# Kernel optimization log

Measured on AMD Instinct MI355X. Metric: run time of the kernel, lower is better.

Reference implementation:

```python
import jax, jax.numpy as jnp
import numpy as np

HALF_FEATURE_NUMEL = 49152  # 12 pieces * 64 squares * 64 king buckets
INTER_DIM = 768             # factorizer collapses king bucket: i % 768


def setup_inputs() -> dict:
    key = jax.random.key(0)
    k1, k2, k3, k4 = jax.random.split(key, 4)
    N = 16384
    nnz = N * 32  # ~32 active features per position
    batch_idx = jnp.sort(jax.random.randint(k1, (nnz,), 0, N, dtype=jnp.int64 if jax.config.read('jax_enable_x64') else jnp.int32))
    active_idx = jax.random.randint(k2, (nnz,), 0, HALF_FEATURE_NUMEL)
    values = jax.random.uniform(k3, (nnz,), dtype=jnp.float32)
    # factorization table self.f = [func(i) for i in range(half_feature_numel)]
    f_table = jnp.arange(HALF_FEATURE_NUMEL) % INTER_DIM
    weights = jax.random.normal(k4, (INTER_DIM, 256), dtype=jnp.float32) * 0.01
    return {"batch_idx": batch_idx, "active_idx": active_idx, "values": values,
            "f_table": f_table, "weights": weights, "N": N}


def reference(batch_idx, active_idx, values, f_table, weights, N):
    # gather: remap active feature ids through factorization table
    factored = f_table[active_idx]                      # [nnz]
    inter_dim = weights.shape[0]
    # scatter-sum duplicates into dense [N, inter_dim] (== sparse COO .to_dense())
    x = jnp.zeros((N, inter_dim), dtype=values.dtype)
    x = x.at[batch_idx, factored].add(values)
    # dense matmul with factored weights
    return x @ weights                                  # [N, output_dim]
```

## Files before the change

kernel.cpp:

```cpp
#include <hip/hip_runtime.h>


#define OUT_COLS 256
#define WAVES_PER_BLOCK 4
#define BLOCK_THREADS (WAVES_PER_BLOCK * 64)
#define NW (768 * 256)

__device__ __forceinline__ float bf2f(unsigned u) {
    return __int_as_float((int)(u << 16));
}
__device__ __forceinline__ unsigned f2bf(float x) {
    unsigned u = __float_as_uint(x);
    return (u + 0x7fffu + ((u >> 16) & 1u)) >> 16;
}

__global__ __launch_bounds__(256)
void conv_kernel(const float* __restrict__ w, unsigned short* __restrict__ wbf, int n) {
    const int i = blockIdx.x * 256 + threadIdx.x;
    if (i < n) wbf[i] = (unsigned short)f2bf(w[i]);
}

__global__ __launch_bounds__(256)
void build_kernel(const int* __restrict__ batch_idx,
                  const int* __restrict__ active_idx,
                  const float* __restrict__ values,
                  const int* __restrict__ f_table,
                  int* __restrict__ offsets,
                  unsigned* __restrict__ pairs,
                  int nnz, int N)
{
    const int k = blockIdx.x * blockDim.x + threadIdx.x;
    if (k >= nnz) return;
    const int r  = batch_idx[k];
    const int rp = (k == 0) ? -1 : batch_idx[k - 1];
    for (int row = rp + 1; row <= r; ++row) offsets[row] = k;
    if (k == nnz - 1)
        for (int row = r + 1; row <= N; ++row) offsets[row] = nnz;
    const unsigned f = (unsigned)f_table[active_idx[k]];
    pairs[k] = (f << 16) | f2bf(values[k]);
}

__global__ __launch_bounds__(BLOCK_THREADS, 8)
void gemm_kernel(const int* __restrict__ offsets,
                 const unsigned* __restrict__ pairs,
                 const unsigned short* __restrict__ wbf,
                 float* __restrict__ out, int N)
{
    const int lane = threadIdx.x & 63;
    const int row  = blockIdx.x * WAVES_PER_BLOCK + (threadIdx.x >> 6);
    if (row >= N) return;

    const int start = __builtin_amdgcn_readfirstlane(offsets[row]);
    const int end   = __builtin_amdgcn_readfirstlane(offsets[row + 1]);

    float4 acc = make_float4(0.f, 0.f, 0.f, 0.f);
    const unsigned short* __restrict__ wbase = wbf + (lane << 2);

    int k = start;
    for (; k + 16 <= end; k += 16) {
        unsigned p[16];
#pragma unroll
        for (int j = 0; j < 16; ++j) p[j] = pairs[k + j];
        ushort4 w[16];
#pragma unroll
        for (int j = 0; j < 16; ++j)
            w[j] = *(const ushort4*)(wbase + (p[j] >> 16) * OUT_COLS);
#pragma unroll
        for (int j = 0; j < 16; ++j) {
            const float v = bf2f(p[j] & 0xffffu);
            acc.x = fmaf(v, bf2f(w[j].x), acc.x);
            acc.y = fmaf(v, bf2f(w[j].y), acc.y);
            acc.z = fmaf(v, bf2f(w[j].z), acc.z);
            acc.w = fmaf(v, bf2f(w[j].w), acc.w);
        }
    }
    for (; k < end; ++k) {
        const unsigned p = pairs[k];
        const float v = bf2f(p & 0xffffu);
        const ushort4 w = *(const ushort4*)(wbase + (p >> 16) * OUT_COLS);
        acc.x = fmaf(v, bf2f(w.x), acc.x);
        acc.y = fmaf(v, bf2f(w.y), acc.y);
        acc.z = fmaf(v, bf2f(w.z), acc.z);
        acc.w = fmaf(v, bf2f(w.w), acc.w);
    }

    *(float4*)(out + row * OUT_COLS + (lane << 2)) = acc;
}

__global__ __launch_bounds__(256, 8)
void fallback_kernel(const int* __restrict__ batch_idx,
                     const int* __restrict__ active_idx,
                     const float* __restrict__ values,
                     const int* __restrict__ f_table,
                     const float* __restrict__ weights,
                     float* __restrict__ out,
                     int nnz, int N)
{
    const int wave = threadIdx.x >> 6;
    const int lane = threadIdx.x & 63;
    const int row  = blockIdx.x * 4 + wave;
    if (row >= N) return;

    int lo1 = 0, hi1 = nnz, lo2 = 0, hi2 = nnz;
    while ((lo1 < hi1) | (lo2 < hi2)) {
        if (lo1 < hi1) { int m = (lo1 + hi1) >> 1; if (batch_idx[m] < row) lo1 = m + 1; else hi1 = m; }
        if (lo2 < hi2) { int m = (lo2 + hi2) >> 1; if (batch_idx[m] < row + 1) lo2 = m + 1; else hi2 = m; }
    }
    float4 acc = make_float4(0.f, 0.f, 0.f, 0.f);
    const float* __restrict__ wcol = weights + (lane << 2);
    for (int base = lo1; base < lo2; base += 64) {
        const int cnt = min(lo2 - base, 64);
        float v_l = 0.f; int f_l = 0;
        if (lane < cnt) { const int k = base + lane; v_l = values[k]; f_l = f_table[active_idx[k]]; }
        for (int j = 0; j < cnt; ++j) {
            const float v = __shfl(v_l, j);
            const int   f = __shfl(f_l, j);
            const float4 w = *(const float4*)(wcol + f * OUT_COLS);
            acc.x = fmaf(v, w.x, acc.x);
            acc.y = fmaf(v, w.y, acc.y);
            acc.z = fmaf(v, w.z, acc.z);
            acc.w = fmaf(v, w.w, acc.w);
        }
    }
    *(float4*)(out + row * OUT_COLS + (lane << 2)) = acc;
}

extern "C" void kernel_launch(void* const* d_in, const int* in_sizes, int n_in,
                              void* d_out, int out_size, void* d_ws, size_t ws_size,
                              hipStream_t stream) {
    const int*   batch_idx  = (const int*)d_in[0];
    const int*   active_idx = (const int*)d_in[1];
    const float* values     = (const float*)d_in[2];
    const int*   f_table    = (const int*)d_in[3];
    const float* weights    = (const float*)d_in[4];
    float*       out        = (float*)d_out;

    const int nnz = in_sizes[0];
    const int N   = out_size / OUT_COLS;

    const size_t off_bytes = (size_t)(N + 1) * sizeof(int);
    const size_t wbf_off   = (off_bytes + 15) & ~(size_t)15;
    const size_t pairs_off = (wbf_off + (size_t)NW * 2 + 15) & ~(size_t)15;
    const size_t need      = pairs_off + (size_t)nnz * sizeof(unsigned);

    const int grid_rows = (N + WAVES_PER_BLOCK - 1) / WAVES_PER_BLOCK;

    if (ws_size >= need) {
        int*            offsets = (int*)d_ws;
        unsigned short* wbf     = (unsigned short*)((char*)d_ws + wbf_off);
        unsigned*       pairs   = (unsigned*)((char*)d_ws + pairs_off);

        conv_kernel<<<(NW + 255) / 256, 256, 0, stream>>>(weights, wbf, NW);
        build_kernel<<<(nnz + 255) / 256, 256, 0, stream>>>(
            batch_idx, active_idx, values, f_table, offsets, pairs, nnz, N);
        gemm_kernel<<<grid_rows, BLOCK_THREADS, 0, stream>>>(offsets, pairs, wbf, out, N);
    } else {
        fallback_kernel<<<grid_rows, 256, 0, stream>>>(
            batch_idx, active_idx, values, f_table, weights, out, nnz, N);
    }
}
```

Baseline: 95.98 us.

## Switch gather-GEMM to fp16 packed FMA with half-wave split and fused conversion

Weights and values are converted to fp16 instead of bf16, and the weight conversion is folded into the build kernel, which removes one launch. The gemm kernel splits each wave into two halves that each take alternate nonzeros, load 8 halfs per lane and accumulate with packed half2 FMAs. The halves are combined with a cross-half shuffle before the store. This halves the number of FMA instructions and merges the tail loop into masked 16-wide chunks, at the cost of fp16 accumulation precision and overflow risk.

Result: faster. 89.28 us (-7.0%).

```diff
diff --git a/kernel.cpp b/kernel.cpp
--- a/kernel.cpp
+++ b/kernel.cpp
@@ -1,4 +1,5 @@
 #include <hip/hip_runtime.h>
+#include <hip/hip_fp16.h>
 
 
 #define OUT_COLS 256
@@ -6,30 +7,19 @@
 #define BLOCK_THREADS (WAVES_PER_BLOCK * 64)
 #define NW (768 * 256)
 
-__device__ __forceinline__ float bf2f(unsigned u) {
-    return __int_as_float((int)(u << 16));
-}
-__device__ __forceinline__ unsigned f2bf(float x) {
-    unsigned u = __float_as_uint(x);
-    return (u + 0x7fffu + ((u >> 16) & 1u)) >> 16;
-}
-
-__global__ __launch_bounds__(256)
-void conv_kernel(const float* __restrict__ w, unsigned short* __restrict__ wbf, int n) {
-    const int i = blockIdx.x * 256 + threadIdx.x;
-    if (i < n) wbf[i] = (unsigned short)f2bf(w[i]);
-}
-
 __global__ __launch_bounds__(256)
 void build_kernel(const int* __restrict__ batch_idx,
                   const int* __restrict__ active_idx,
                   const float* __restrict__ values,
                   const int* __restrict__ f_table,
+                  const float* __restrict__ weights,
                   int* __restrict__ offsets,
                   unsigned* __restrict__ pairs,
+                  __half* __restrict__ wh,
                   int nnz, int N)
 {
-    const int k = blockIdx.x * blockDim.x + threadIdx.x;
+    const int k = blockIdx.x * 256 + threadIdx.x;
+    if (k < NW) wh[k] = __float2half(weights[k]);
     if (k >= nnz) return;
     const int r  = batch_idx[k];
     const int rp = (k == 0) ? -1 : batch_idx[k - 1];
@@ -37,13 +27,13 @@
     if (k == nnz - 1)
         for (int row = r + 1; row <= N; ++row) offsets[row] = nnz;
     const unsigned f = (unsigned)f_table[active_idx[k]];
-    pairs[k] = (f << 16) | f2bf(values[k]);
+    pairs[k] = (f << 16) | (unsigned)__half_as_ushort(__float2half(values[k]));
 }
 
 __global__ __launch_bounds__(BLOCK_THREADS, 8)
 void gemm_kernel(const int* __restrict__ offsets,
                  const unsigned* __restrict__ pairs,
-                 const unsigned short* __restrict__ wbf,
+                 const __half* __restrict__ wh,
                  float* __restrict__ out, int N)
 {
     const int lane = threadIdx.x & 63;
@@ -53,38 +43,58 @@
     const int start = __builtin_amdgcn_readfirstlane(offsets[row]);
     const int end   = __builtin_amdgcn_readfirstlane(offsets[row + 1]);
 
-    float4 acc = make_float4(0.f, 0.f, 0.f, 0.f);
-    const unsigned short* __restrict__ wbase = wbf + (lane << 2);
+    const __half2 zero = __float2half2_rn(0.0f);
+    __half2 acc0 = zero, acc1 = zero, acc2 = zero, acc3 = zero;
 
-    int k = start;
-    for (; k + 16 <= end; k += 16) {
+    const __half* __restrict__ wbase = wh + ((lane & 31) << 3);
+    const bool lo_half = (lane < 32);
+
+    for (int k = start; k < end; k += 16) {
         unsigned p[16];
 #pragma unroll
-        for (int j = 0; j < 16; ++j) p[j] = pairs[k + j];
-        ushort4 w[16];
+        for (int j = 0; j < 16; ++j) {
+            const unsigned raw = pairs[k + j];
+            p[j] = (k + j < end) ? raw : 0u;
+        }
+        uint4 w[8];
 #pragma unroll
-        for (int j = 0; j < 16; ++j)
-            w[j] = *(const ushort4*)(wbase + (p[j] >> 16) * OUT_COLS);
+        for (int b = 0; b < 8; ++b) {
+            const int f0 = (int)(p[2 * b] >> 16);
+            const int f1 = (int)(p[2 * b + 1] >> 16);
+            const int f  = lo_half ? f0 : f1;
+            w[b] = *(const uint4*)(wbase + (f << 8));
+        }
 #pragma unroll
-        for (int j = 0; j < 16; ++j) {
-            const float v = bf2f(p[j] & 0xffffu);
-            acc.x = fmaf(v, bf2f(w[j].x), acc.x);
-            acc.y = fmaf(v, bf2f(w[j].y), acc.y);
-            acc.z = fmaf(v, bf2f(w[j].z), acc.z);
-            acc.w = fmaf(v, bf2f(w[j].w), acc.w);
+        for (int b = 0; b < 8; ++b) {
+            unsigned vv0 = p[2 * b] & 0xffffu;       vv0 |= vv0 << 16;
+            unsigned vv1 = p[2 * b + 1] & 0xffffu;   vv1 |= vv1 << 16;
+            const unsigned vvu = lo_half ? vv0 : vv1;
+            const __half2 vv = *(const __half2*)&vvu;
+            const __half2* w2 = (const __half2*)&w[b];
+            acc0 = __hfma2(w2[0], vv, acc0);
+            acc1 = __hfma2(w2[1], vv, acc1);
+            acc2 = __hfma2(w2[2], vv, acc2);
+            acc3 = __hfma2(w2[3], vv, acc3);
         }
     }
-    for (; k < end; ++k) {
-        const unsigned p = pairs[k];
-        const float v = bf2f(p & 0xffffu);
-        const ushort4 w = *(const ushort4*)(wbase + (p >> 16) * OUT_COLS);
-        acc.x = fmaf(v, bf2f(w.x), acc.x);
-        acc.y = fmaf(v, bf2f(w.y), acc.y);
-        acc.z = fmaf(v, bf2f(w.z), acc.z);
-        acc.w = fmaf(v, bf2f(w.w), acc.w);
+
+    __half2 accs[4] = {acc0, acc1, acc2, acc3};
+#pragma unroll
+    for (int i = 0; i < 4; ++i) {
+        int a = *(const int*)&accs[i];
+        const int b = __shfl_xor(a, 32);
+        accs[i] = __hadd2(accs[i], *(const __half2*)&b);
     }
-
-    *(float4*)(out + row * OUT_COLS + (lane << 2)) = acc;
+    if (lo_half) {
+        float4 o0, o1;
+        o0.x = __low2float(accs[0]); o0.y = __high2float(accs[0]);
+        o0.z = __low2float(accs[1]); o0.w = __high2float(accs[1]);
+        o1.x = __low2float(accs[2]); o1.y = __high2float(accs[2]);
+        o1.z = __low2float(accs[3]); o1.w = __high2float(accs[3]);
+        float* orow = out + row * OUT_COLS + (lane << 3);
+        *(float4*)orow = o0;
+        *(float4*)(orow + 4) = o1;
+    }
 }
 
 __global__ __launch_bounds__(256, 8)
@@ -139,21 +149,22 @@
     const int N   = out_size / OUT_COLS;
 
     const size_t off_bytes = (size_t)(N + 1) * sizeof(int);
-    const size_t wbf_off   = (off_bytes + 15) & ~(size_t)15;
-    const size_t pairs_off = (wbf_off + (size_t)NW * 2 + 15) & ~(size_t)15;
-    const size_t need      = pairs_off + (size_t)nnz * sizeof(unsigned);
+    const size_t wh_off    = (off_bytes + 15) & ~(size_t)15;
+    const size_t pairs_off = (wh_off + (size_t)NW * 2 + 15) & ~(size_t)15;
+    const size_t need      = pairs_off + (size_t)nnz * sizeof(unsigned) + 64;
 
     const int grid_rows = (N + WAVES_PER_BLOCK - 1) / WAVES_PER_BLOCK;
 
     if (ws_size >= need) {
-        int*            offsets = (int*)d_ws;
-        unsigned short* wbf     = (unsigned short*)((char*)d_ws + wbf_off);
-        unsigned*       pairs   = (unsigned*)((char*)d_ws + pairs_off);
+        int*      offsets = (int*)d_ws;
+        __half*   wh      = (__half*)((char*)d_ws + wh_off);
+        unsigned* pairs   = (unsigned*)((char*)d_ws + pairs_off);
 
-        conv_kernel<<<(NW + 255) / 256, 256, 0, stream>>>(weights, wbf, NW);
-        build_kernel<<<(nnz + 255) / 256, 256, 0, stream>>>(
-            batch_idx, active_idx, values, f_table, offsets, pairs, nnz, N);
-        gemm_kernel<<<grid_rows, BLOCK_THREADS, 0, stream>>>(offsets, pairs, wbf, out, N);
+        const int work = (nnz > NW) ? nnz : NW;
+        build_kernel<<<(work + 255) / 256, 256, 0, stream>>>(
+            batch_idx, active_idx, values, f_table, weights,
+            offsets, pairs, wh, nnz, N);
+        gemm_kernel<<<grid_rows, BLOCK_THREADS, 0, stream>>>(offsets, pairs, wh, out, N);
     } else {
         fallback_kernel<<<grid_rows, 256, 0, stream>>>(
             batch_idx, active_idx, values, f_table, weights, out, nnz, N);
```
